# Optimization experiments

Hardware: AMD Instinct MI355X
Metric: run time of the kernel (lower is better)

Reference implementation:

```python
import jax, jax.numpy as jnp
import numpy as np

QB = 127.0  # 2**(8-1) - 1


def ternary_dequant(w):
    # absmean ternary quantization, then dequantize by scale
    scale = jnp.mean(jnp.abs(w))
    w_t = jnp.clip(jnp.round(w / (scale + 1e-8)), -1.0, 1.0)
    w_t = jnp.where(scale == 0.0, jnp.zeros_like(w), w_t)
    return w_t * scale


def activation_quantize(x):
    # per-row (last-dim) absmax int8 fake-quant
    scale = jnp.max(jnp.abs(x), axis=-1, keepdims=True) / QB
    scale = jnp.maximum(scale, 1e-8)
    return jnp.clip(jnp.round(x / scale), -QB, QB) * scale


def setup_inputs() -> dict:
    key = jax.random.key(0)
    kx, kw = jax.random.split(key)
    x = jax.random.normal(kx, (2, 4096, 4096), dtype=jnp.float32)
    # kaiming_uniform-ish init scale; exact init distribution is irrelevant to the math
    bound = 1.0 / np.sqrt(4096)
    weight = jax.random.uniform(kw, (4096, 4096), dtype=jnp.float32,
                                minval=-bound, maxval=bound)
    return {"x": x, "weight": weight}


def reference(x, weight):
    w_q = ternary_dequant(weight)        # [out, in]
    x_q = activation_quantize(x)         # [b, s, in]
    return jnp.einsum('bsi,oi->bso', x_q, w_q)
```

## Files before the change

### kernel.cpp

```cpp
#include <hip/hip_runtime.h>
#include <stdint.h>
#include <stddef.h>


#define K_DIM 4096
#define M_DIM 8192
#define N_DIM 4096

typedef int v4i __attribute__((ext_vector_type(4)));

__device__ __forceinline__ void async_copy16(void* lds, const void* g) {
  __builtin_amdgcn_global_load_lds(
      (const __attribute__((address_space(1))) unsigned int*)g,
      (__attribute__((address_space(3))) unsigned int*)lds,
      16, 0, 0);
}

__global__ void k_wsum(const float* __restrict__ w, double* __restrict__ partials) {
  const float4* w4 = (const float4*)w;
  int tid = blockIdx.x * 256 + threadIdx.x;
  double s = 0.0;
  for (int i = tid; i < 4194304; i += 262144) {
    float4 v = w4[i];
    s += (double)fabsf(v.x) + (double)fabsf(v.y) +
         (double)fabsf(v.z) + (double)fabsf(v.w);
  }
  for (int off = 32; off > 0; off >>= 1) s += __shfl_down(s, off);
  __shared__ double lsum[4];
  int lane = threadIdx.x & 63, wid = threadIdx.x >> 6;
  if (lane == 0) lsum[wid] = s;
  __syncthreads();
  if (threadIdx.x == 0)
    partials[blockIdx.x] = lsum[0] + lsum[1] + lsum[2] + lsum[3];
}

__global__ void k_wscale(const double* __restrict__ partials, float* __restrict__ wscale) {
  double s = 0.0;
  for (int i = threadIdx.x; i < 1024; i += 256) s += partials[i];
  for (int off = 32; off > 0; off >>= 1) s += __shfl_down(s, off);
  __shared__ double lsum[4];
  int lane = threadIdx.x & 63, wid = threadIdx.x >> 6;
  if (lane == 0) lsum[wid] = s;
  __syncthreads();
  if (threadIdx.x == 0) {
    double tot = lsum[0] + lsum[1] + lsum[2] + lsum[3];
    *wscale = (float)(tot / 16777216.0);
  }
}

__global__ void k_wq(const float* __restrict__ w, const float* __restrict__ wscale,
                     char* __restrict__ qw) {
  float d = *wscale + 1e-8f;
  const float4* w4 = (const float4*)w;
  int* q4 = (int*)qw;
  int tid = blockIdx.x * 256 + threadIdx.x;
  for (int i = tid; i < 4194304; i += 524288) {
    float4 v = w4[i];
    int a = (int)fmaxf(fminf(rintf(v.x / d), 1.f), -1.f);
    int b = (int)fmaxf(fminf(rintf(v.y / d), 1.f), -1.f);
    int c = (int)fmaxf(fminf(rintf(v.z / d), 1.f), -1.f);
    int e = (int)fmaxf(fminf(rintf(v.w / d), 1.f), -1.f);
    q4[i] = (a & 255) | ((b & 255) << 8) | ((c & 255) << 16) | ((e & 255) << 24);
  }
}

__global__ void k_xq(const float* __restrict__ x, char* __restrict__ qx,
                     float* __restrict__ sx) {
  int row = blockIdx.x;
  const float4* xr = (const float4*)(x + (size_t)row * K_DIM);
  float4 v[4];
  float m = 0.f;
#pragma unroll
  for (int c = 0; c < 4; c++) {
    v[c] = xr[threadIdx.x + c * 256];
    m = fmaxf(m, fmaxf(fmaxf(fabsf(v[c].x), fabsf(v[c].y)),
                       fmaxf(fabsf(v[c].z), fabsf(v[c].w))));
  }
  for (int off = 32; off > 0; off >>= 1) m = fmaxf(m, __shfl_down(m, off));
  __shared__ float lm[4];
  __shared__ float bscale;
  int lane = threadIdx.x & 63, wid = threadIdx.x >> 6;
  if (lane == 0) lm[wid] = m;
  __syncthreads();
  if (threadIdx.x == 0) {
    float mm = fmaxf(fmaxf(lm[0], lm[1]), fmaxf(lm[2], lm[3]));
    float sc = fmaxf(mm / 127.0f, 1e-8f);
    bscale = sc;
    sx[row] = sc;
  }
  __syncthreads();
  float sc = bscale;
  int* q4 = (int*)(qx + (size_t)row * K_DIM);
#pragma unroll
  for (int c = 0; c < 4; c++) {
    int a = (int)fmaxf(fminf(rintf(v[c].x / sc), 127.f), -127.f);
    int b = (int)fmaxf(fminf(rintf(v[c].y / sc), 127.f), -127.f);
    int cc = (int)fmaxf(fminf(rintf(v[c].z / sc), 127.f), -127.f);
    int e = (int)fmaxf(fminf(rintf(v[c].w / sc), 127.f), -127.f);
    q4[threadIdx.x + c * 256] = (a & 255) | ((b & 255) << 8) | ((cc & 255) << 16) | ((e & 255) << 24);
  }
}

__global__ void k_gemm(const char* __restrict__ qx, const char* __restrict__ qw,
                       const float* __restrict__ sx, const float* __restrict__ wscale,
                       float* __restrict__ out) {
  __shared__ char ldsA[128 * 64];
  __shared__ char ldsB[128 * 64];

  const int bn = blockIdx.x & 31;
  const int bm = blockIdx.x >> 5;
  const int rowBase = bm * 128;
  const int colBase = bn * 128;
  const int tid = threadIdx.x;
  const int lane = tid & 63;
  const int wave = tid >> 6;
  const int wr = wave >> 1, wc = wave & 1;

  v4i acc[4][4] = {};

  const int sRow = wave * 32 + (lane >> 2);
  const int sK = (lane & 3) * 16;
  const char* gA0 = qx + (size_t)(rowBase + sRow) * K_DIM + sK;
  const char* gA1 = gA0 + 16 * K_DIM;
  const char* gB0 = qw + (size_t)(colBase + sRow) * K_DIM + sK;
  const char* gB1 = gB0 + 16 * K_DIM;
  char* lA0 = ldsA + wave * 2048;
  char* lA1 = lA0 + 1024;
  char* lB0 = ldsB + wave * 2048;
  char* lB1 = lB0 + 1024;

  const int kseg = (lane >> 4) * 16;
  const char* aPtr = ldsA + (wr * 64 + (lane & 15)) * 64 + kseg;
  const char* bPtr = ldsB + (wc * 64 + (lane & 15)) * 64 + kseg;

  for (int kb = 0; kb < K_DIM / 64; kb++) {
    if (kb) __syncthreads();
    const int goff = kb * 64;
    async_copy16(lA0, gA0 + goff);
    async_copy16(lA1, gA1 + goff);
    async_copy16(lB0, gB0 + goff);
    async_copy16(lB1, gB1 + goff);
    __syncthreads();

    v4i a[4], b[4];
#pragma unroll
    for (int t = 0; t < 4; t++) {
      a[t] = *(const v4i*)(aPtr + t * 16 * 64);
      b[t] = *(const v4i*)(bPtr + t * 16 * 64);
    }
#pragma unroll
    for (int mt = 0; mt < 4; mt++)
#pragma unroll
      for (int nt = 0; nt < 4; nt++)
        acc[mt][nt] = __builtin_amdgcn_mfma_i32_16x16x64_i8(a[mt], b[nt], acc[mt][nt], 0, 0, 0);
  }

  const float sw = *wscale;
  const int col0 = colBase + wc * 64 + (lane & 15);
  const int row0 = rowBase + wr * 64 + (lane >> 4) * 4;
#pragma unroll
  for (int mt = 0; mt < 4; mt++) {
#pragma unroll
    for (int r = 0; r < 4; r++) {
      const int row = row0 + mt * 16 + r;
      const float s = sx[row] * sw;
#pragma unroll
      for (int nt = 0; nt < 4; nt++)
        out[(size_t)row * N_DIM + col0 + nt * 16] = (float)acc[mt][nt][r] * s;
    }
  }
}

extern "C" void kernel_launch(void* const* d_in, const int* in_sizes, int n_in,
                              void* d_out, int out_size, void* d_ws, size_t ws_size,
                              hipStream_t stream) {
  const float* x = (const float*)d_in[0];
  const float* w = (const float*)d_in[1];
  float* out = (float*)d_out;
  char* ws = (char*)d_ws;

  double* partials = (double*)ws;
  float* wscale    = (float*)(ws + 8192);
  float* sx        = (float*)(ws + 8448);
  char*  qw        = ws + 41472;
  char*  qx        = ws + 41472 + 16777216;

  k_wsum  <<<1024, 256, 0, stream>>>(w, partials);
  k_wscale<<<   1, 256, 0, stream>>>(partials, wscale);
  k_wq    <<<2048, 256, 0, stream>>>(w, wscale, qw);
  k_xq    <<<8192, 256, 0, stream>>>(x, qx, sx);
  k_gemm  <<<64 * 32, 256, 0, stream>>>(qx, qw, sx, wscale, out);
}
```

Measured before the change: 423.8 us.

## Rewrite int8 GEMM with 256x256 tiles and 4-stage async LDS pipeline

The int8 MFMA GEMM moves from 128x128 tiles with 256 threads and a single LDS buffer to 256x256 tiles with 512 threads. It adds a four-buffer ring of async global-to-LDS copies, kept three stages ahead and governed by explicit vmcnt waits and barriers, so loads overlap with MFMA work. It also adds an XOR swizzle on the k-segment to reduce LDS bank conflicts, a remapping of block indices to group tiles, and setprio around the MFMA loop. In exchange it uses 128KB of LDS per block, which limits each CU to a single resident block, and raises register pressure from 32 accumulators per lane.

```diff
diff --git a/kernel.cpp b/kernel.cpp
--- a/kernel.cpp
+++ b/kernel.cpp
@@ -101,72 +101,96 @@
   }
 }
 
-__global__ void k_gemm(const char* __restrict__ qx, const char* __restrict__ qw,
-                       const float* __restrict__ sx, const float* __restrict__ wscale,
+__global__ __launch_bounds__(512, 2) void k_gemm(const char* __restrict__ qx,
+                       const char* __restrict__ qw,
+                       const float* __restrict__ sx,
+                       const float* __restrict__ wscale,
                        float* __restrict__ out) {
-  __shared__ char ldsA[128 * 64];
-  __shared__ char ldsB[128 * 64];
-
-  const int bn = blockIdx.x & 31;
-  const int bm = blockIdx.x >> 5;
-  const int rowBase = bm * 128;
-  const int colBase = bn * 128;
+  __shared__ char lds[4][32768];
+
   const int tid = threadIdx.x;
   const int lane = tid & 63;
   const int wave = tid >> 6;
-  const int wr = wave >> 1, wc = wave & 1;
-
-  v4i acc[4][4] = {};
-
-  const int sRow = wave * 32 + (lane >> 2);
-  const int sK = (lane & 3) * 16;
-  const char* gA0 = qx + (size_t)(rowBase + sRow) * K_DIM + sK;
-  const char* gA1 = gA0 + 16 * K_DIM;
-  const char* gB0 = qw + (size_t)(colBase + sRow) * K_DIM + sK;
-  const char* gB1 = gB0 + 16 * K_DIM;
-  char* lA0 = ldsA + wave * 2048;
-  char* lA1 = lA0 + 1024;
-  char* lB0 = ldsB + wave * 2048;
-  char* lB1 = lB0 + 1024;
-
-  const int kseg = (lane >> 4) * 16;
-  const char* aPtr = ldsA + (wr * 64 + (lane & 15)) * 64 + kseg;
-  const char* bPtr = ldsB + (wc * 64 + (lane & 15)) * 64 + kseg;
-
-  for (int kb = 0; kb < K_DIM / 64; kb++) {
-    if (kb) __syncthreads();
-    const int goff = kb * 64;
-    async_copy16(lA0, gA0 + goff);
-    async_copy16(lA1, gA1 + goff);
-    async_copy16(lB0, gB0 + goff);
-    async_copy16(lB1, gB1 + goff);
-    __syncthreads();
-
-    v4i a[4], b[4];
-#pragma unroll
-    for (int t = 0; t < 4; t++) {
-      a[t] = *(const v4i*)(aPtr + t * 16 * 64);
-      b[t] = *(const v4i*)(bPtr + t * 16 * 64);
+  const int wr = wave >> 2;
+  const int wc = wave & 3;
+
+  const int wg = (blockIdx.x & 7) * 64 + (blockIdx.x >> 3);
+  const int bm = wg >> 4;
+  const int bn = wg & 15;
+  const int rowBase = bm * 256;
+  const int colBase = bn * 256;
+
+  const int rl = tid >> 2;
+  const int kswz = (((tid & 3) ^ ((rl >> 1) & 3)) << 4);
+  const char* gA0 = qx + (size_t)(rowBase + rl) * K_DIM + kswz;
+  const char* gA1 = gA0 + (size_t)128 * K_DIM;
+  const char* gB0 = qw + (size_t)(colBase + rl) * K_DIM + kswz;
+  const char* gB1 = gB0 + (size_t)128 * K_DIM;
+  const int dOff = wave << 10;
+
+  const int sR = ((lane & 15) >> 1) & 3;
+  const int kro = (((lane >> 4) ^ sR) << 4);
+  const int aOff = ((wr << 7) + (lane & 15)) * 64 + kro;
+  const int bOff = 16384 + ((wc << 6) + (lane & 15)) * 64 + kro;
+
+  v4i acc[8][4] = {};
+
+  auto STAGE = [&](int t) {
+    char* b = &lds[t & 3][0];
+    const size_t ko = (size_t)t << 6;
+    async_copy16(b + dOff,         gA0 + ko);
+    async_copy16(b + 8192 + dOff,  gA1 + ko);
+    async_copy16(b + 16384 + dOff, gB0 + ko);
+    async_copy16(b + 24576 + dOff, gB1 + ko);
+  };
+
+  auto COMPUTE = [&](int t) {
+    const char* b = &lds[t & 3][0];
+    v4i bf[4];
+#pragma unroll
+    for (int n = 0; n < 4; ++n)
+      bf[n] = *(const v4i*)(b + bOff + n * 1024);
+    __builtin_amdgcn_s_setprio(1);
+#pragma unroll
+    for (int m = 0; m < 8; ++m) {
+      v4i af = *(const v4i*)(b + aOff + m * 1024);
+#pragma unroll
+      for (int n = 0; n < 4; ++n)
+        acc[m][n] = __builtin_amdgcn_mfma_i32_16x16x64_i8(af, bf[n], acc[m][n], 0, 0, 0);
     }
-#pragma unroll
-    for (int mt = 0; mt < 4; mt++)
-#pragma unroll
-      for (int nt = 0; nt < 4; nt++)
-        acc[mt][nt] = __builtin_amdgcn_mfma_i32_16x16x64_i8(a[mt], b[nt], acc[mt][nt], 0, 0, 0);
-  }
-
-  const float sw = *wscale;
-  const int col0 = colBase + wc * 64 + (lane & 15);
-  const int row0 = rowBase + wr * 64 + (lane >> 4) * 4;
-#pragma unroll
-  for (int mt = 0; mt < 4; mt++) {
-#pragma unroll
-    for (int r = 0; r < 4; r++) {
-      const int row = row0 + mt * 16 + r;
-      const float s = sx[row] * sw;
-#pragma unroll
-      for (int nt = 0; nt < 4; nt++)
-        out[(size_t)row * N_DIM + col0 + nt * 16] = (float)acc[mt][nt][r] * s;
+    __builtin_amdgcn_s_setprio(0);
+  };
+
+  STAGE(0); STAGE(1); STAGE(2);
+
+  for (int t = 0; t < 61; ++t) {
+    asm volatile("s_waitcnt vmcnt(8)" ::: "memory");
+    __builtin_amdgcn_s_barrier();
+    STAGE(t + 3);
+    COMPUTE(t);
+  }
+  asm volatile("s_waitcnt vmcnt(8)" ::: "memory");
+  __builtin_amdgcn_s_barrier();
+  COMPUTE(61);
+  asm volatile("s_waitcnt vmcnt(4)" ::: "memory");
+  __builtin_amdgcn_s_barrier();
+  COMPUTE(62);
+  asm volatile("s_waitcnt vmcnt(0)" ::: "memory");
+  __builtin_amdgcn_s_barrier();
+  COMPUTE(63);
+
+  const float swv = *wscale;
+  const int col0 = colBase + (wc << 6) + (lane & 15);
+  const int row0 = rowBase + (wr << 7) + ((lane >> 4) << 2);
+#pragma unroll
+  for (int m = 0; m < 8; ++m) {
+#pragma unroll
+    for (int r = 0; r < 4; ++r) {
+      const int row = row0 + m * 16 + r;
+      const float s = sx[row] * swv;
+#pragma unroll
+      for (int n = 0; n < 4; ++n)
+        out[(size_t)row * N_DIM + col0 + n * 16] = (float)acc[m][n][r] * s;
     }
   }
 }
@@ -189,5 +213,5 @@
   k_wscale<<<   1, 256, 0, stream>>>(partials, wscale);
   k_wq    <<<2048, 256, 0, stream>>>(w, wscale, qw);
   k_xq    <<<8192, 256, 0, stream>>>(x, qx, sx);
-  k_gemm  <<<64 * 32, 256, 0, stream>>>(qx, qw, sx, wscale, out);
-}
+  k_gemm  <<<32 * 16, 512, 0, stream>>>(qx, qw, sx, wscale, out);
+}
```

After: 394.6 us. -6.9%, faster.
